# Kernel optimization log

Hardware: AMD Instinct MI355X
Metric: run time of the kernel (lower is better)

Reference implementation:

```python
import jax, jax.numpy as jnp
import numpy as np

B, T, D, H = 64, 512, 512, 1024


def setup_inputs() -> dict:
    key = jax.random.key(0)
    k1, k2 = jax.random.split(key, 2)
    x = jax.random.normal(k1, (B, T, D), dtype=jnp.float32)
    W = jax.random.normal(k2, (D, H), dtype=jnp.float32) * 0.02
    b = jnp.zeros((H,), dtype=jnp.float32)
    return {"x": x, "W": W, "b": b}


def reference(x, W, b):
    # Step model (docstring example of RecurrentWrapper):
    #   h_new = sigmoid(h + relu(x_t @ W + b))
    # The Dense projection is time-independent, so hoist it out of the scan
    # (same math as applying it per step inside tf.scan).
    proj = jax.nn.relu(jnp.einsum('btd,dh->bth', x, W) + b)  # [B,T,H]
    proj_t = jnp.swapaxes(proj, 0, 1)  # [T,B,H], matches _swap_time_and_samples
    h0 = jnp.zeros((x.shape[0], W.shape[1]), dtype=x.dtype)  # zeros initial state

    def step(h, p_t):
        h_new = jax.nn.sigmoid(h + p_t)
        return h_new, h_new

    _, hs = jax.lax.scan(step, h0, proj_t)  # [T,B,H]
    return jnp.swapaxes(hs, 0, 1)  # [B,T,H] (return_sequences=True)
```

## Files before the change

### kernel.cpp

```cpp
#include <hip/hip_runtime.h>
#include <hip/hip_bf16.h>
#include <stdint.h>

#define B_ 64
#define T_ 512
#define D_ 512
#define H_ 1024
#define M_ (B_*T_)
#define K_ D_
#define N_ H_

#define BM 128
#define BN 128
#define BK 64
#define NKT (K_/BK)

typedef __attribute__((ext_vector_type(4))) float f32x4;
typedef __attribute__((ext_vector_type(8))) short s16x8;
typedef __attribute__((ext_vector_type(4))) short s16x4;
typedef unsigned short u16;

__device__ __forceinline__ short f2bf(float f) {
  __bf16 h = (__bf16)f;
  return __builtin_bit_cast(short, h);
}
__device__ __forceinline__ float bf2f(u16 u) {
  return __builtin_bit_cast(float, ((unsigned)u) << 16);
}
__device__ __forceinline__ s16x4 cvt4(f32x4 v) {
  s16x4 r;
  r[0] = f2bf(v[0]); r[1] = f2bf(v[1]);
  r[2] = f2bf(v[2]); r[3] = f2bf(v[3]);
  return r;
}
__device__ __forceinline__ void gload_lds16(const void* g, void* l) {
  __builtin_amdgcn_global_load_lds(
      (const __attribute__((address_space(1))) void*)g,
      (__attribute__((address_space(3))) void*)l, 16, 0, 0);
}


__global__ __launch_bounds__(256)
void cvt_x(const float* __restrict__ x, u16* __restrict__ xb) {
  const int stride = gridDim.x * blockDim.x;
  const int nvec = M_ * K_ / 8;
  for (int i = blockIdx.x * blockDim.x + threadIdx.x; i < nvec; i += stride) {
    f32x4 a = ((const f32x4*)x)[2*i];
    f32x4 b = ((const f32x4*)x)[2*i + 1];
    s16x8 r;
    r[0]=f2bf(a[0]); r[1]=f2bf(a[1]); r[2]=f2bf(a[2]); r[3]=f2bf(a[3]);
    r[4]=f2bf(b[0]); r[5]=f2bf(b[1]); r[6]=f2bf(b[2]); r[7]=f2bf(b[3]);
    ((s16x8*)xb)[i] = r;
  }
}

__global__ __launch_bounds__(256)
void cvt_wt(const float* __restrict__ W, u16* __restrict__ wt) {
  __shared__ u16 Lt[64 * 72];
  const int n0 = blockIdx.x * 64;
  const int k0 = blockIdx.y * 64;
  const int tid = threadIdx.x;
  #pragma unroll
  for (int p = 0; p < 16; ++p) {
    const int idx = p * 256 + tid;
    const int r = idx >> 6;
    const int c = idx & 63;
    const float v = W[(size_t)(k0 + r) * H_ + n0 + c];
    Lt[c * 72 + r] = (u16)f2bf(v);
  }
  __syncthreads();
  #pragma unroll
  for (int p = 0; p < 2; ++p) {
    const int idx = p * 256 + tid;
    const int rn = idx >> 3;
    const int ck = (idx & 7) * 8;
    const s16x8 v = *(const s16x8*)&Lt[rn * 72 + ck];
    *(s16x8*)&wt[(size_t)(n0 + rn) * K_ + k0 + ck] = v;
  }
}

__global__ __launch_bounds__(256, 2)
void fused_gemm_scan(const u16* __restrict__ xb, const u16* __restrict__ wt,
                     const float* __restrict__ bias, float* __restrict__ out) {
  __shared__ char Asm[BM * BK * 2];
  __shared__ char Bsm[BN * BK * 2];
  __shared__ char Pt[BM * BN * 2];

  const int tid  = threadIdx.x;
  const int lane = tid & 63;
  const int wave = tid >> 6;

  const int rb  = blockIdx.x;
  const int xcd = rb & 7;
  const int idx = rb >> 3;
  const int b   = xcd * 8 + (idx & 7);
  const int ht  = idx >> 3;
  const int n0  = ht * BN;

  const int g  = lane >> 4;
  const int lr = lane & 15;
  const int wr = wave >> 1;
  const int wc = wave & 1;
  const int rSub = lane >> 3;
  const int ke   = (lane & 7) * 8;

  float bv[4];
  #pragma unroll
  for (int n = 0; n < 4; ++n)
    bv[n] = bias[n0 + wc*64 + n*16 + lr];

  const int hcol = tid;
  float hh = 0.f;

  #pragma unroll 1
  for (int tc = 0; tc < 4; ++tc) {
    const int m0 = b * T_ + tc * BM;

    f32x4 acc[4][4];
    #pragma unroll
    for (int m = 0; m < 4; ++m)
      #pragma unroll
      for (int n = 0; n < 4; ++n)
        acc[m][n] = (f32x4){0.f, 0.f, 0.f, 0.f};

    #pragma unroll 1
    for (int kt = 0; kt < NKT; ++kt) {
      if (kt) __syncthreads();
      const int k0 = kt * BK;
      #pragma unroll
      for (int p = 0; p < 4; ++p) {
        const int slot = wave * 4 + p;
        const int r = slot * 8 + rSub;
        gload_lds16(xb + (size_t)(m0 + r) * K_ + k0 + ke, Asm + slot * 1024);
        gload_lds16(wt + (size_t)(n0 + r) * K_ + k0 + ke, Bsm + slot * 1024);
      }
      __syncthreads();

      #pragma unroll
      for (int kk = 0; kk < BK; kk += 32) {
        s16x8 af[4], bf[4];
        #pragma unroll
        for (int m = 0; m < 4; ++m)
          af[m] = *(const s16x8*)(Asm + (wr*64 + m*16 + lr) * 128 + kk*2 + g*16);
        #pragma unroll
        for (int n = 0; n < 4; ++n)
          bf[n] = *(const s16x8*)(Bsm + (wc*64 + n*16 + lr) * 128 + kk*2 + g*16);
        #pragma unroll
        for (int m = 0; m < 4; ++m)
          #pragma unroll
          for (int n = 0; n < 4; ++n)
            acc[m][n] = __builtin_amdgcn_mfma_f32_16x16x32_bf16(
                af[m], bf[n], acc[m][n], 0, 0, 0);
      }
    }

    #pragma unroll
    for (int m = 0; m < 4; ++m) {
      #pragma unroll
      for (int n = 0; n < 4; ++n) {
        const int col2 = (wc*64 + n*16 + lr) * 2;
        #pragma unroll
        for (int j = 0; j < 4; ++j) {
          const int row = wr*64 + m*16 + g*4 + j;
          *(u16*)(Pt + row*256 + (col2 ^ (((row>>2)&7) << 5))) =
              (u16)f2bf(fmaxf(acc[m][n][j] + bv[n], 0.f));
        }
      }
    }
    __syncthreads();

    if (tid < 128) {
      float* o = out + (size_t)(b * T_ + tc * BM) * H_ + n0 + hcol;
      const int c2 = hcol * 2;
      #pragma unroll 8
      for (int t = 0; t < BM; ++t) {
        const float v = bf2f(*(const u16*)(Pt + t*256 + (c2 ^ (((t>>2)&7) << 5))));
        hh = __builtin_amdgcn_rcpf(1.f + __expf(-(hh + v)));
        o[(size_t)t * H_] = hh;
      }
    }
    __syncthreads();
  }
}


__global__ __launch_bounds__(256, 2)
void gemm_bias_relu(const float* __restrict__ X, const float* __restrict__ W,
                    const float* __restrict__ bias, float* __restrict__ out) {
  __shared__ char Asm[BM*BK*2];
  __shared__ char Bsm[BN*BK*2];

  const int tid  = threadIdx.x;
  const int lane = tid & 63;
  const int wave = tid >> 6;
  const int m0 = blockIdx.x * BM;
  const int n0 = blockIdx.y * BN;

  const int arow  = tid >> 4;
  const int acol4 = (tid & 15) << 2;
  const int brow  = tid >> 5;
  const int bn4   = (tid & 31) << 2;

  const int g  = lane >> 4;
  const int lr = lane & 15;
  const int wr = wave >> 1;
  const int wc = wave & 1;

  s16x4 aRegs[8], bRegs[8];
  f32x4 acc[4][4];
  #pragma unroll
  for (int m = 0; m < 4; ++m)
    #pragma unroll
    for (int n = 0; n < 4; ++n)
      acc[m][n] = (f32x4){0.f, 0.f, 0.f, 0.f};

  auto loadTile = [&](int kt) {
    const int k0 = kt * BK;
    #pragma unroll
    for (int p = 0; p < 8; ++p) {
      const int r = p*16 + arow;
      f32x4 av = *(const f32x4*)(X + (size_t)(m0 + r)*K_ + k0 + acol4);
      aRegs[p] = cvt4(av);
      const int kk = p*8 + brow;
      f32x4 bv = *(const f32x4*)(W + (size_t)(k0 + kk)*N_ + n0 + bn4);
      bRegs[p] = cvt4(bv);
    }
  };
  auto writeTile = [&]() {
    #pragma unroll
    for (int p = 0; p < 8; ++p) {
      const int r = p*16 + arow;
      const int ao = ((r*BK + acol4) * 2) ^ ((r & 7) << 4);
      *(s16x4*)(Asm + ao) = aRegs[p];
      const int kk = p*8 + brow;
      #pragma unroll
      for (int i = 0; i < 4; ++i) {
        const int n = bn4 + i;
        const int bo = ((n*BK + kk) * 2) ^ ((n & 7) << 4);
        *(short*)(Bsm + bo) = bRegs[p][i];
      }
    }
  };
  auto mfmaTile = [&]() {
    #pragma unroll
    for (int kk = 0; kk < BK; kk += 32) {
      s16x8 af[4], bf[4];
      #pragma unroll
      for (int m = 0; m < 4; ++m) {
        const int r = wr*64 + m*16 + lr;
        af[m] = *(const s16x8*)(Asm + (((r*BK + kk + g*8) * 2) ^ ((r & 7) << 4)));
      }
      #pragma unroll
      for (int n = 0; n < 4; ++n) {
        const int c = wc*64 + n*16 + lr;
        bf[n] = *(const s16x8*)(Bsm + (((c*BK + kk + g*8) * 2) ^ ((c & 7) << 4)));
      }
      #pragma unroll
      for (int m = 0; m < 4; ++m)
        #pragma unroll
        for (int n = 0; n < 4; ++n)
          acc[m][n] = __builtin_amdgcn_mfma_f32_16x16x32_bf16(
              af[m], bf[n], acc[m][n], 0, 0, 0);
    }
  };

  loadTile(0);
  #pragma unroll 1
  for (int kt = 0; kt < NKT; ++kt) {
    if (kt) __syncthreads();
    writeTile();
    __syncthreads();
    if (kt + 1 < NKT) loadTile(kt + 1);
    mfmaTile();
  }

  float bv[4];
  #pragma unroll
  for (int n = 0; n < 4; ++n)
    bv[n] = bias[n0 + wc*64 + n*16 + lr];
  #pragma unroll
  for (int m = 0; m < 4; ++m)
    #pragma unroll
    for (int n = 0; n < 4; ++n) {
      const int col = n0 + wc*64 + n*16 + lr;
      #pragma unroll
      for (int j = 0; j < 4; ++j) {
        const int row = m0 + wr*64 + m*16 + g*4 + j;
        out[(size_t)row*N_ + col] = fmaxf(acc[m][n][j] + bv[n], 0.f);
      }
    }
}

#define PF 16
__global__ __launch_bounds__(256)
void scan_sigmoid(float* __restrict__ out) {
  const int tid = blockIdx.x * blockDim.x + threadIdx.x;
  const int b = tid >> 10;
  const int h = tid & (H_ - 1);
  float* p = out + (size_t)b * (T_ * H_) + h;

  float buf[PF];
  #pragma unroll
  for (int i = 0; i < PF; ++i) buf[i] = p[(size_t)i * H_];

  float hh = 0.f;
  #pragma unroll 1
  for (int t0 = 0; t0 < T_ - PF; t0 += PF) {
    #pragma unroll
    for (int i = 0; i < PF; ++i) {
      const float v = buf[i];
      buf[i] = p[(size_t)(t0 + i + PF) * H_];
      hh = __builtin_amdgcn_rcpf(1.f + __expf(-(hh + v)));
      p[(size_t)(t0 + i) * H_] = hh;
    }
  }
  #pragma unroll
  for (int i = 0; i < PF; ++i) {
    const float v = buf[i];
    hh = __builtin_amdgcn_rcpf(1.f + __expf(-(hh + v)));
    p[(size_t)(T_ - PF + i) * H_] = hh;
  }
}


extern "C" void kernel_launch(void* const* d_in, const int* in_sizes, int n_in,
                              void* d_out, int out_size, void* d_ws, size_t ws_size,
                              hipStream_t stream) {
  const float* x    = (const float*)d_in[0];
  const float* W    = (const float*)d_in[1];
  const float* bias = (const float*)d_in[2];
  float* out = (float*)d_out;

  const size_t XB = (size_t)M_ * K_ * 2;
  const size_t WT = (size_t)N_ * K_ * 2;

  if (ws_size >= XB + WT) {
    u16* xb = (u16*)d_ws;
    u16* wt = (u16*)((char*)d_ws + XB);

    cvt_x<<<2048, 256, 0, stream>>>(x, xb);
    cvt_wt<<<dim3(N_/64, K_/64), 256, 0, stream>>>(W, wt);
    fused_gemm_scan<<<B_ * (N_/BN), 256, 0, stream>>>(xb, wt, bias, out);
  } else {
    gemm_bias_relu<<<dim3(M_/BM, N_/BN), 256, 0, stream>>>(x, W, bias, out);
    scan_sigmoid<<<(B_*H_)/256, 256, 0, stream>>>(out);
  }
}
```

Measured before the change: 96.85 us.

## Swizzle GEMM LDS tiles to avoid bank conflicts and merge prep kernels

The two conversion kernels (x to bf16, W transpose to bf16) are merged into one launch, with the first 128 blocks handling W and the rest handling x. In the fused GEMM+scan kernel, the global-to-LDS loads now write XOR-swizzled 16-byte chunks, and the fragment reads apply the matching XOR so that the 128-byte LDS rows no longer cause bank conflicts. The A and B loads are also split into separate loops. This saves one launch and reduces LDS bank conflicts, at the cost of extra index arithmetic.

```diff
diff --git a/kernel.cpp b/kernel.cpp
--- a/kernel.cpp
+++ b/kernel.cpp
@@ -11,9 +11,11 @@
 #define N_ H_
 
 #define BM 128
-#define BN 128
+#define BNF 128
 #define BK 64
 #define NKT (K_/BK)
+
+#define BN 128
 
 typedef __attribute__((ext_vector_type(4))) float f32x4;
 typedef __attribute__((ext_vector_type(8))) short s16x8;
@@ -41,41 +43,42 @@
 
 
 __global__ __launch_bounds__(256)
-void cvt_x(const float* __restrict__ x, u16* __restrict__ xb) {
-  const int stride = gridDim.x * blockDim.x;
-  const int nvec = M_ * K_ / 8;
-  for (int i = blockIdx.x * blockDim.x + threadIdx.x; i < nvec; i += stride) {
-    f32x4 a = ((const f32x4*)x)[2*i];
-    f32x4 b = ((const f32x4*)x)[2*i + 1];
-    s16x8 r;
-    r[0]=f2bf(a[0]); r[1]=f2bf(a[1]); r[2]=f2bf(a[2]); r[3]=f2bf(a[3]);
-    r[4]=f2bf(b[0]); r[5]=f2bf(b[1]); r[6]=f2bf(b[2]); r[7]=f2bf(b[3]);
-    ((s16x8*)xb)[i] = r;
-  }
-}
-
-__global__ __launch_bounds__(256)
-void cvt_wt(const float* __restrict__ W, u16* __restrict__ wt) {
+void prep(const float* __restrict__ x, const float* __restrict__ W,
+          u16* __restrict__ xb, u16* __restrict__ wt) {
   __shared__ u16 Lt[64 * 72];
-  const int n0 = blockIdx.x * 64;
-  const int k0 = blockIdx.y * 64;
   const int tid = threadIdx.x;
-  #pragma unroll
-  for (int p = 0; p < 16; ++p) {
-    const int idx = p * 256 + tid;
-    const int r = idx >> 6;
-    const int c = idx & 63;
-    const float v = W[(size_t)(k0 + r) * H_ + n0 + c];
-    Lt[c * 72 + r] = (u16)f2bf(v);
-  }
-  __syncthreads();
-  #pragma unroll
-  for (int p = 0; p < 2; ++p) {
-    const int idx = p * 256 + tid;
-    const int rn = idx >> 3;
-    const int ck = (idx & 7) * 8;
-    const s16x8 v = *(const s16x8*)&Lt[rn * 72 + ck];
-    *(s16x8*)&wt[(size_t)(n0 + rn) * K_ + k0 + ck] = v;
+
+  if (blockIdx.x < 128) {
+    const int n0 = (blockIdx.x & 15) * 64;
+    const int k0 = (blockIdx.x >> 4) * 64;
+    #pragma unroll
+    for (int p = 0; p < 16; ++p) {
+      const int idx = p * 256 + tid;
+      const int r = idx >> 6;
+      const int c = idx & 63;
+      const float v = W[(size_t)(k0 + r) * H_ + n0 + c];
+      Lt[c * 72 + r] = (u16)f2bf(v);
+    }
+    __syncthreads();
+    #pragma unroll
+    for (int p = 0; p < 2; ++p) {
+      const int idx = p * 256 + tid;
+      const int rn = idx >> 3;
+      const int ck = (idx & 7) * 8;
+      const s16x8 v = *(const s16x8*)&Lt[rn * 72 + ck];
+      *(s16x8*)&wt[(size_t)(n0 + rn) * K_ + k0 + ck] = v;
+    }
+  } else {
+    const int nvec = M_ * K_ / 8;
+    const int stride = 2048 * 256;
+    for (int i = (blockIdx.x - 128) * 256 + tid; i < nvec; i += stride) {
+      f32x4 a = ((const f32x4*)x)[2*i];
+      f32x4 b = ((const f32x4*)x)[2*i + 1];
+      s16x8 r;
+      r[0]=f2bf(a[0]); r[1]=f2bf(a[1]); r[2]=f2bf(a[2]); r[3]=f2bf(a[3]);
+      r[4]=f2bf(b[0]); r[5]=f2bf(b[1]); r[6]=f2bf(b[2]); r[7]=f2bf(b[3]);
+      ((s16x8*)xb)[i] = r;
+    }
   }
 }
 
@@ -83,8 +86,8 @@
 void fused_gemm_scan(const u16* __restrict__ xb, const u16* __restrict__ wt,
                      const float* __restrict__ bias, float* __restrict__ out) {
   __shared__ char Asm[BM * BK * 2];
-  __shared__ char Bsm[BN * BK * 2];
-  __shared__ char Pt[BM * BN * 2];
+  __shared__ char Bsm[BNF * BK * 2];
+  __shared__ char Pt[BM * BNF * 2];
 
   const int tid  = threadIdx.x;
   const int lane = tid & 63;
@@ -95,14 +98,14 @@
   const int idx = rb >> 3;
   const int b   = xcd * 8 + (idx & 7);
   const int ht  = idx >> 3;
-  const int n0  = ht * BN;
+  const int n0  = ht * BNF;
 
   const int g  = lane >> 4;
   const int lr = lane & 15;
   const int wr = wave >> 1;
   const int wc = wave & 1;
   const int rSub = lane >> 3;
-  const int ke   = (lane & 7) * 8;
+  const int kec  = ((lane & 7) ^ rSub) * 8;
 
   float bv[4];
   #pragma unroll
@@ -131,8 +134,13 @@
       for (int p = 0; p < 4; ++p) {
         const int slot = wave * 4 + p;
         const int r = slot * 8 + rSub;
-        gload_lds16(xb + (size_t)(m0 + r) * K_ + k0 + ke, Asm + slot * 1024);
-        gload_lds16(wt + (size_t)(n0 + r) * K_ + k0 + ke, Bsm + slot * 1024);
+        gload_lds16(xb + (size_t)(m0 + r) * K_ + k0 + kec, Asm + slot * 1024);
+      }
+      #pragma unroll
+      for (int p = 0; p < 4; ++p) {
+        const int slot = wave * 4 + p;
+        const int r = slot * 8 + rSub;
+        gload_lds16(wt + (size_t)(n0 + r) * K_ + k0 + kec, Bsm + slot * 1024);
       }
       __syncthreads();
 
@@ -140,11 +148,17 @@
       for (int kk = 0; kk < BK; kk += 32) {
         s16x8 af[4], bf[4];
         #pragma unroll
-        for (int m = 0; m < 4; ++m)
-          af[m] = *(const s16x8*)(Asm + (wr*64 + m*16 + lr) * 128 + kk*2 + g*16);
-        #pragma unroll
-        for (int n = 0; n < 4; ++n)
-          bf[n] = *(const s16x8*)(Bsm + (wc*64 + n*16 + lr) * 128 + kk*2 + g*16);
+        for (int m = 0; m < 4; ++m) {
+          const int row = wr*64 + m*16 + lr;
+          af[m] = *(const s16x8*)(Asm + row*128 +
+                                  ((kk*2 + g*16) ^ ((row & 7) << 4)));
+        }
+        #pragma unroll
+        for (int n = 0; n < 4; ++n) {
+          const int row = wc*64 + n*16 + lr;
+          bf[n] = *(const s16x8*)(Bsm + row*128 +
+                                  ((kk*2 + g*16) ^ ((row & 7) << 4)));
+        }
         #pragma unroll
         for (int m = 0; m < 4; ++m)
           #pragma unroll
@@ -338,9 +352,8 @@
     u16* xb = (u16*)d_ws;
     u16* wt = (u16*)((char*)d_ws + XB);
 
-    cvt_x<<<2048, 256, 0, stream>>>(x, xb);
-    cvt_wt<<<dim3(N_/64, K_/64), 256, 0, stream>>>(W, wt);
-    fused_gemm_scan<<<B_ * (N_/BN), 256, 0, stream>>>(xb, wt, bias, out);
+    prep<<<2176, 256, 0, stream>>>(x, W, xb, wt);
+    fused_gemm_scan<<<B_ * (N_/BNF), 256, 0, stream>>>(xb, wt, bias, out);
   } else {
     gemm_bias_relu<<<dim3(M_/BM, N_/BN), 256, 0, stream>>>(x, W, bias, out);
     scan_sigmoid<<<(B_*H_)/256, 256, 0, stream>>>(out);
```

New measurement: 84.51 us. -12.7%, faster.
